# Kernel optimization log

Measured on AMD Instinct MI355X. Metric: run time of the kernel, lower is better.

The kernel has to match this reference:

```python
import jax, jax.numpy as jnp
from jax import lax
import numpy as np

DIVISOR = 2.0

def setup_inputs() -> dict:
    key = jax.random.key(0)
    k1, k2, k3, k4 = jax.random.split(key, 4)
    B, Cin, D, H, W = 64, 8, 32, 64, 64
    Cout, KD, KH, KW = 16, 3, 3, 3
    fan_in = Cin * KD * KH * KW
    bound = 1.0 / np.sqrt(fan_in)
    x = jax.random.normal(k1, (B, Cin, D, H, W), dtype=jnp.float32)
    conv_weight = jax.random.uniform(k2, (Cout, Cin, KD, KH, KW), jnp.float32, -bound, bound)
    conv_bias = jax.random.uniform(k3, (Cout,), jnp.float32, -bound, bound)
    bias = jax.random.normal(k4, (Cout, 1, 1, 1), dtype=jnp.float32) * 0.02
    return {"x": x, "conv_weight": conv_weight, "conv_bias": conv_bias, "bias": bias}

def reference(x, conv_weight, conv_bias, bias):
    # Conv3d, stride 1, no padding, groups=1  -> [B, Cout, D-2, H-2, W-2]
    y = lax.conv_general_dilated(
        x, conv_weight, window_strides=(1, 1, 1), padding='VALID',
        dimension_numbers=('NCDHW', 'OIDHW', 'NCDHW'))
    y = y + conv_bias[None, :, None, None, None]
    # Divide by constant
    y = y / DIVISOR
    # MaxPool3d(kernel=2, stride=2), floor mode (VALID drops the trailing odd row)
    y = lax.reduce_window(y, -jnp.inf, lax.max,
                          window_dimensions=(1, 1, 2, 2, 2),
                          window_strides=(1, 1, 2, 2, 2), padding='VALID')
    # AdaptiveAvgPool3d((1,1,1)) == global mean over spatial dims
    y = jnp.mean(y, axis=(2, 3, 4), keepdims=True)  # [B, Cout, 1, 1, 1]
    # Bias add (broadcast over batch)
    y = y + bias[None]
    # Sum over channel dim (sum_dim=1, no keepdim)
    return jnp.sum(y, axis=1)  # [B, 1, 1, 1]
```

## Files before the change

kernel.cpp:

```cpp
#include <hip/hip_runtime.h>

typedef __attribute__((ext_vector_type(8))) short short8;
typedef __attribute__((ext_vector_type(4))) float f32x4;
typedef unsigned int u32;

#define ROW_B 1056
#define SLOT_B 10560
#define NSLOT 4

__device__ __forceinline__ unsigned short f2bf(float f) {
  unsigned u = __builtin_bit_cast(unsigned, f);
  u += 0x7FFFu + ((u >> 16) & 1u);
  return (unsigned short)(u >> 16);
}
__device__ __forceinline__ u32 cvtpk(float lo, float hi) {
  u32 r;
  asm("v_cvt_pk_bf16_f32 %0, %1, %2" : "=v"(r) : "v"(lo), "v"(hi));
  return r;
}

#define MF(ACC, H, FR, KD, KH)                                                \
  ACC[H][wt] = __builtin_amdgcn_mfma_f32_16x16x32_bf16(FR, bfragB[KD][KH],    \
                                                       ACC[H][wt], 0, 0, 0)
#define MFI(ACC, H, FR)                                                       \
  ACC[H][wt] = __builtin_amdgcn_mfma_f32_16x16x32_bf16(FR, bfragB[0][0],      \
                                                       zf4, 0, 0, 0)

#define PROC(DP, AN, AM, AO, K1, K2, DOCLOSE, SAVEP, DOSTAGE)                 \
  {                                                                           \
    const int dp_ = (DP);                                                     \
    if (DOSTAGE) {                                                            \
      stage_load(dp_ + 2);                                                    \
      __builtin_amdgcn_sched_barrier(0);     \
    }                                                                         \
    const int sb_ = (dp_ & 3) * SLOT_B + rowbase;                             \
    __builtin_amdgcn_s_setprio(1);                                            \
    _Pragma("unroll") for (int wt = 0; wt < 4; ++wt) {                        \
      const short8 f0 = *(const short8*)(smem + sb_ + 0 * ROW_B + physoff[wt]); \
      const short8 f1 = *(const short8*)(smem + sb_ + 1 * ROW_B + physoff[wt]); \
      const short8 f2 = *(const short8*)(smem + sb_ + 2 * ROW_B + physoff[wt]); \
      const short8 f3 = *(const short8*)(smem + sb_ + 3 * ROW_B + physoff[wt]); \
      MFI(AN, 0, f0); MFI(AN, 1, f1);                                         \
      MF(AN, 0, f1, 0, 1); MF(AN, 1, f2, 0, 1);                               \
      MF(AN, 0, f2, 0, 2); MF(AN, 1, f3, 0, 2);                               \
      if (K1) {                                                               \
        MF(AM, 0, f0, 1, 0); MF(AM, 1, f1, 1, 0);                             \
        MF(AM, 0, f1, 1, 1); MF(AM, 1, f2, 1, 1);                             \
        MF(AM, 0, f2, 1, 2); MF(AM, 1, f3, 1, 2);                             \
      }                                                                       \
      if (K2) {                                                               \
        MF(AO, 0, f0, 2, 0); MF(AO, 1, f1, 2, 0);                             \
        MF(AO, 0, f1, 2, 1); MF(AO, 1, f2, 2, 1);                             \
        MF(AO, 0, f2, 2, 2); MF(AO, 1, f3, 2, 2);                             \
      }                                                                       \
    }                                                                         \
    __builtin_amdgcn_s_setprio(0);                                            \
    if (DOSTAGE) stage_write(dp_ + 2);                                        \
    __syncthreads();                                                          \
    if (DOCLOSE) {                                                            \
      _Pragma("unroll") for (int wt = 0; wt < 4; ++wt) {                      \
        const float e01 = fmaxf(fmaxf(AO[0][wt][0], AO[0][wt][1]),            \
                                fmaxf(AO[1][wt][0], AO[1][wt][1]));           \
        const float e23 = fmaxf(fmaxf(AO[0][wt][2], AO[0][wt][3]),            \
                                fmaxf(AO[1][wt][2], AO[1][wt][3]));           \
        if (SAVEP) {                                                          \
          p01[wt] = e01; p23[wt] = e23;                                       \
        } else if (hvalid) {                                                  \
          sum += fmaxf(p01[wt], e01);                                         \
          if (!(wt == 3 && g == 3)) sum += fmaxf(p23[wt], e23);               \
        }                                                                     \
      }                                                                       \
    }                                                                         \
  }

__launch_bounds__(256, 2)
__global__ void conv_fused(const float* __restrict__ x,
                           const float* __restrict__ cw,
                           float* __restrict__ ws) {
  __shared__ __align__(16) unsigned char smem[NSLOT * SLOT_B];
  __shared__ float wsum[4];

  const int bid = blockIdx.x;
  const int b   = bid >> 3;
  const int hq  = bid & 7;
  const int h0  = hq * 8;

  const int tid  = threadIdx.x;
  const int lane = tid & 63;
  const int wid  = tid >> 6;
  const int nm   = lane & 15;
  const int g    = lane >> 4;

  const float* xb = x + (size_t)b * (8u * 32u * 64u * 64u);

  short8 bfragB[3][3];
#pragma unroll
  for (int kd = 0; kd < 3; ++kd)
#pragma unroll
    for (int kh = 0; kh < 3; ++kh) {
      short8 f;
#pragma unroll
      for (int j = 0; j < 8; ++j) {
        float v = (g < 3) ? cw[(nm * 8 + j) * 27 + kd * 9 + kh * 3 + g] : 0.f;
        f[j] = (short)f2bf(v);
      }
      bfragB[kd][kh] = f;
    }

  const int gc = (g < 3) ? g : 2;
  int physoff[4];
#pragma unroll
  for (int wt = 0; wt < 4; ++wt) physoff[wt] = (wt * 16 + nm + gc) * 16;
  const int rowbase = (2 * wid) * ROW_B;

  bool st_act[3]; const float* st_base[3]; int st_off[3];
#pragma unroll
  for (int pass = 0; pass < 3; ++pass) {
    const int t = tid + pass * 256;
    bool act = (t < 640);
    int row = (t >> 6) % 10;
    const int w = t & 63;
    int h = h0 + row;
    if (h > 63) { act = false; h = 63; }
    st_act[pass]  = act;
    st_base[pass] = xb + h * 64 + w;
    st_off[pass]  = row * ROW_B + w * 16;
  }

  float ld[3][8];

  auto stage_load = [&](int p) {
#pragma unroll
    for (int pass = 0; pass < 3; ++pass) {
      if (st_act[pass]) {
        const float* sp = st_base[pass] + p * 4096;
#pragma unroll
        for (int c = 0; c < 8; ++c) ld[pass][c] = sp[(size_t)c * 131072];
      }
    }
  };
  auto stage_write = [&](int p) {
    unsigned char* d = smem + (p & 3) * SLOT_B;
#pragma unroll
    for (int pass = 0; pass < 3; ++pass) {
      if (st_act[pass]) {
        uint4 v;
        v.x = cvtpk(ld[pass][0], ld[pass][1]);
        v.y = cvtpk(ld[pass][2], ld[pass][3]);
        v.z = cvtpk(ld[pass][4], ld[pass][5]);
        v.w = cvtpk(ld[pass][6], ld[pass][7]);
        *(uint4*)(d + st_off[pass]) = v;
      }
    }
  };

  const bool hvalid = !(hq == 7 && wid == 3);
  const f32x4 zf4 = {0.f, 0.f, 0.f, 0.f};
  float sum = 0.f;
  float p01[4], p23[4];
  f32x4 accA[2][4], accB[2][4], accC[2][4];

  stage_load(0); stage_write(0);
  stage_load(1); stage_write(1);
  __syncthreads();

  PROC(0, accA, accB, accC, 0, 0, 0, 0, 1)
  PROC(1, accB, accA, accC, 1, 0, 0, 0, 1)

  for (int p0 = 2; p0 <= 20; p0 += 6) {
    PROC(p0 + 0, accC, accB, accA, 1, 1, 1, 1, 1)
    PROC(p0 + 1, accA, accC, accB, 1, 1, 1, 0, 1)
    PROC(p0 + 2, accB, accA, accC, 1, 1, 1, 1, 1)
    PROC(p0 + 3, accC, accB, accA, 1, 1, 1, 0, 1)
    PROC(p0 + 4, accA, accC, accB, 1, 1, 1, 1, 1)
    PROC(p0 + 5, accB, accA, accC, 1, 1, 1, 0, 1)
  }
  PROC(26, accC, accB, accA, 1, 1, 1, 1, 1)
  PROC(27, accA, accC, accB, 1, 1, 1, 0, 1)
  PROC(28, accB, accA, accC, 1, 1, 1, 1, 1)
  PROC(29, accC, accB, accA, 1, 1, 1, 0, 1)
  PROC(30, accA, accC, accB, 1, 1, 1, 1, 0)
  PROC(31, accB, accA, accC, 1, 1, 1, 0, 0)

#pragma unroll
  for (int off = 32; off > 0; off >>= 1) sum += __shfl_down(sum, off);
  if (lane == 0) wsum[wid] = sum;
  __syncthreads();
  if (tid == 0) ws[bid] = wsum[0] + wsum[1] + wsum[2] + wsum[3];
}

__global__ void finalize_k(const float* __restrict__ ws,
                           const float* __restrict__ cb,
                           const float* __restrict__ bias,
                           float* __restrict__ out) {
  const int b = threadIdx.x;
  float s = 0.f;
#pragma unroll
  for (int hq = 0; hq < 8; ++hq) s += ws[b * 8 + hq];
  float cbs = 0.f, bs = 0.f;
#pragma unroll
  for (int c = 0; c < 16; ++c) { cbs += cb[c]; bs += bias[c]; }
  out[b] = 0.5f * s / 14415.f + 0.5f * cbs + bs;
}

extern "C" void kernel_launch(void* const* d_in, const int* in_sizes, int n_in,
                              void* d_out, int out_size, void* d_ws, size_t ws_size,
                              hipStream_t stream) {
  const float* x    = (const float*)d_in[0];
  const float* cw   = (const float*)d_in[1];
  const float* cb   = (const float*)d_in[2];
  const float* bias = (const float*)d_in[3];
  float* out = (float*)d_out;
  float* ws  = (float*)d_ws;

  hipLaunchKernelGGL(conv_fused, dim3(512), dim3(256), 0, stream, x, cw, ws);
  hipLaunchKernelGGL(finalize_k, dim3(1), dim3(64), 0, stream, ws, cb, bias, out);
}
```

Baseline: 75.28 us.

## Split conv tile into half-height blocks with 2x2 wave layout and fewer barriers

```diff
diff --git a/kernel.cpp b/kernel.cpp
--- a/kernel.cpp
+++ b/kernel.cpp
@@ -5,7 +5,7 @@
 typedef unsigned int u32;
 
 #define ROW_B 1056
-#define SLOT_B 10560
+#define SLOT_B 6336
 #define NSLOT 4
 
 __device__ __forceinline__ unsigned short f2bf(float f) {
@@ -26,16 +26,13 @@
   ACC[H][wt] = __builtin_amdgcn_mfma_f32_16x16x32_bf16(FR, bfragB[0][0],      \
                                                        zf4, 0, 0, 0)
 
-#define PROC(DP, AN, AM, AO, K1, K2, DOCLOSE, SAVEP, DOSTAGE)                 \
+#define PROC(DP, AN, AM, AO, K1, K2, DOCLOSE, SAVEP, DOSTAGE, DOBAR)          \
   {                                                                           \
     const int dp_ = (DP);                                                     \
-    if (DOSTAGE) {                                                            \
-      stage_load(dp_ + 2);                                                    \
-      __builtin_amdgcn_sched_barrier(0);     \
-    }                                                                         \
+    if (DOSTAGE) stage(dp_ + 2);                                              \
     const int sb_ = (dp_ & 3) * SLOT_B + rowbase;                             \
     __builtin_amdgcn_s_setprio(1);                                            \
-    _Pragma("unroll") for (int wt = 0; wt < 4; ++wt) {                        \
+    _Pragma("unroll") for (int wt = 0; wt < 2; ++wt) {                        \
       const short8 f0 = *(const short8*)(smem + sb_ + 0 * ROW_B + physoff[wt]); \
       const short8 f1 = *(const short8*)(smem + sb_ + 1 * ROW_B + physoff[wt]); \
       const short8 f2 = *(const short8*)(smem + sb_ + 2 * ROW_B + physoff[wt]); \
@@ -55,41 +52,42 @@
       }                                                                       \
     }                                                                         \
     __builtin_amdgcn_s_setprio(0);                                            \
-    if (DOSTAGE) stage_write(dp_ + 2);                                        \
-    __syncthreads();                                                          \
+    if (DOBAR) __syncthreads();                                               \
     if (DOCLOSE) {                                                            \
-      _Pragma("unroll") for (int wt = 0; wt < 4; ++wt) {                      \
+      _Pragma("unroll") for (int wt = 0; wt < 2; ++wt) {                      \
         const float e01 = fmaxf(fmaxf(AO[0][wt][0], AO[0][wt][1]),            \
                                 fmaxf(AO[1][wt][0], AO[1][wt][1]));           \
         const float e23 = fmaxf(fmaxf(AO[0][wt][2], AO[0][wt][3]),            \
                                 fmaxf(AO[1][wt][2], AO[1][wt][3]));           \
         if (SAVEP) {                                                          \
           p01[wt] = e01; p23[wt] = e23;                                       \
-        } else if (hvalid) {                                                  \
+        } else if (pairvalid) {                                               \
           sum += fmaxf(p01[wt], e01);                                         \
-          if (!(wt == 3 && g == 3)) sum += fmaxf(p23[wt], e23);               \
+          if (!(wt == 1 && wmask)) sum += fmaxf(p23[wt], e23);                \
         }                                                                     \
       }                                                                       \
     }                                                                         \
   }
 
-__launch_bounds__(256, 2)
+__launch_bounds__(256, 3)
 __global__ void conv_fused(const float* __restrict__ x,
                            const float* __restrict__ cw,
                            float* __restrict__ ws) {
   __shared__ __align__(16) unsigned char smem[NSLOT * SLOT_B];
   __shared__ float wsum[4];
 
-  const int bid = blockIdx.x;
-  const int b   = bid >> 3;
-  const int hq  = bid & 7;
-  const int h0  = hq * 8;
+  const int rb  = blockIdx.x;
+  const int bid = (rb & 7) * 128 + (rb >> 3);
+  const int b   = bid >> 4;
+  const int hq  = bid & 15;
 
   const int tid  = threadIdx.x;
   const int lane = tid & 63;
   const int wid  = tid >> 6;
   const int nm   = lane & 15;
   const int g    = lane >> 4;
+  const int hp   = wid >> 1;
+  const int wh   = wid & 1;
 
   const float* xb = x + (size_t)b * (8u * 32u * 64u * 64u);
 
@@ -108,82 +106,80 @@
     }
 
   const int gc = (g < 3) ? g : 2;
-  int physoff[4];
-#pragma unroll
-  for (int wt = 0; wt < 4; ++wt) physoff[wt] = (wt * 16 + nm + gc) * 16;
-  const int rowbase = (2 * wid) * ROW_B;
-
-  bool st_act[3]; const float* st_base[3]; int st_off[3];
-#pragma unroll
-  for (int pass = 0; pass < 3; ++pass) {
-    const int t = tid + pass * 256;
-    bool act = (t < 640);
-    int row = (t >> 6) % 10;
-    const int w = t & 63;
-    int h = h0 + row;
-    if (h > 63) { act = false; h = 63; }
-    st_act[pass]  = act;
-    st_base[pass] = xb + h * 64 + w;
-    st_off[pass]  = row * ROW_B + w * 16;
-  }
-
-  float ld[3][8];
-
-  auto stage_load = [&](int p) {
-#pragma unroll
-    for (int pass = 0; pass < 3; ++pass) {
-      if (st_act[pass]) {
-        const float* sp = st_base[pass] + p * 4096;
-#pragma unroll
-        for (int c = 0; c < 8; ++c) ld[pass][c] = sp[(size_t)c * 131072];
-      }
+  int physoff[2];
+#pragma unroll
+  for (int wt = 0; wt < 2; ++wt)
+    physoff[wt] = ((2 * wh + wt) * 16 + nm + gc) * 16;
+  const int rowbase = (2 * hp) * ROW_B;
+
+  const int w0    = tid & 63;
+  const int srow0 = tid >> 6;
+  const int srow1 = 4 + (srow0 & 1);
+  int h0 = 4 * hq + srow0; if (h0 > 63) h0 = 63;
+  int h1 = 4 * hq + srow1; if (h1 > 63) h1 = 63;
+  const float* st_base0 = xb + h0 * 64 + w0;
+  const float* st_base1 = xb + h1 * 64 + w0;
+  const int st_off0 = srow0 * ROW_B + w0 * 16;
+  const int st_off1 = srow1 * ROW_B + w0 * 16;
+  const bool act1 = (tid < 128);
+
+  auto stage = [&](int p) {
+    unsigned char* d = smem + (p & 3) * SLOT_B;
+    {
+      const float* sp = st_base0 + p * 4096;
+      float v[8];
+#pragma unroll
+      for (int c = 0; c < 8; ++c) v[c] = sp[(size_t)c * 131072];
+      uint4 q;
+      q.x = cvtpk(v[0], v[1]); q.y = cvtpk(v[2], v[3]);
+      q.z = cvtpk(v[4], v[5]); q.w = cvtpk(v[6], v[7]);
+      *(uint4*)(d + st_off0) = q;
+    }
+    if (act1) {
+      const float* sp = st_base1 + p * 4096;
+      float v[8];
+#pragma unroll
+      for (int c = 0; c < 8; ++c) v[c] = sp[(size_t)c * 131072];
+      uint4 q;
+      q.x = cvtpk(v[0], v[1]); q.y = cvtpk(v[2], v[3]);
+      q.z = cvtpk(v[4], v[5]); q.w = cvtpk(v[6], v[7]);
+      *(uint4*)(d + st_off1) = q;
     }
   };
-  auto stage_write = [&](int p) {
-    unsigned char* d = smem + (p & 3) * SLOT_B;
-#pragma unroll
-    for (int pass = 0; pass < 3; ++pass) {
-      if (st_act[pass]) {
-        uint4 v;
-        v.x = cvtpk(ld[pass][0], ld[pass][1]);
-        v.y = cvtpk(ld[pass][2], ld[pass][3]);
-        v.z = cvtpk(ld[pass][4], ld[pass][5]);
-        v.w = cvtpk(ld[pass][6], ld[pass][7]);
-        *(uint4*)(d + st_off[pass]) = v;
-      }
-    }
-  };
-
-  const bool hvalid = !(hq == 7 && wid == 3);
+
+  const bool pairvalid = !(hq == 15 && hp == 1);
+  const bool wmask = (wh == 1) && (g == 3);
+
   const f32x4 zf4 = {0.f, 0.f, 0.f, 0.f};
   float sum = 0.f;
-  float p01[4], p23[4];
-  f32x4 accA[2][4], accB[2][4], accC[2][4];
-
-  stage_load(0); stage_write(0);
-  stage_load(1); stage_write(1);
+  float p01[2], p23[2];
+  f32x4 accA[2][2], accB[2][2], accC[2][2];
+
+  stage(0);
+  stage(1);
   __syncthreads();
 
-  PROC(0, accA, accB, accC, 0, 0, 0, 0, 1)
-  PROC(1, accB, accA, accC, 1, 0, 0, 0, 1)
+  PROC(0, accA, accB, accC, 0, 0, 0, 0, 1, 0)
+  PROC(1, accB, accA, accC, 1, 0, 0, 0, 1, 1)
 
   for (int p0 = 2; p0 <= 20; p0 += 6) {
-    PROC(p0 + 0, accC, accB, accA, 1, 1, 1, 1, 1)
-    PROC(p0 + 1, accA, accC, accB, 1, 1, 1, 0, 1)
-    PROC(p0 + 2, accB, accA, accC, 1, 1, 1, 1, 1)
-    PROC(p0 + 3, accC, accB, accA, 1, 1, 1, 0, 1)
-    PROC(p0 + 4, accA, accC, accB, 1, 1, 1, 1, 1)
-    PROC(p0 + 5, accB, accA, accC, 1, 1, 1, 0, 1)
+    PROC(p0 + 0, accC, accB, accA, 1, 1, 1, 1, 1, 0)
+    PROC(p0 + 1, accA, accC, accB, 1, 1, 1, 0, 1, 1)
+    PROC(p0 + 2, accB, accA, accC, 1, 1, 1, 1, 1, 0)
+    PROC(p0 + 3, accC, accB, accA, 1, 1, 1, 0, 1, 1)
+    PROC(p0 + 4, accA, accC, accB, 1, 1, 1, 1, 1, 0)
+    PROC(p0 + 5, accB, accA, accC, 1, 1, 1, 0, 1, 1)
   }
-  PROC(26, accC, accB, accA, 1, 1, 1, 1, 1)
-  PROC(27, accA, accC, accB, 1, 1, 1, 0, 1)
-  PROC(28, accB, accA, accC, 1, 1, 1, 1, 1)
-  PROC(29, accC, accB, accA, 1, 1, 1, 0, 1)
-  PROC(30, accA, accC, accB, 1, 1, 1, 1, 0)
-  PROC(31, accB, accA, accC, 1, 1, 1, 0, 0)
+  PROC(26, accC, accB, accA, 1, 1, 1, 1, 1, 0)
+  PROC(27, accA, accC, accB, 1, 1, 1, 0, 1, 1)
+  PROC(28, accB, accA, accC, 1, 1, 1, 1, 1, 0)
+  PROC(29, accC, accB, accA, 1, 1, 1, 0, 1, 1)
+  PROC(30, accA, accC, accB, 1, 1, 1, 1, 0, 0)
+  PROC(31, accB, accA, accC, 1, 1, 1, 0, 0, 0)
 
 #pragma unroll
   for (int off = 32; off > 0; off >>= 1) sum += __shfl_down(sum, off);
+  __syncthreads();
   if (lane == 0) wsum[wid] = sum;
   __syncthreads();
   if (tid == 0) ws[bid] = wsum[0] + wsum[1] + wsum[2] + wsum[3];
@@ -196,7 +192,7 @@
   const int b = threadIdx.x;
   float s = 0.f;
 #pragma unroll
-  for (int hq = 0; hq < 8; ++hq) s += ws[b * 8 + hq];
+  for (int hq = 0; hq < 16; ++hq) s += ws[b * 16 + hq];
   float cbs = 0.f, bs = 0.f;
 #pragma unroll
   for (int c = 0; c < 16; ++c) { cbs += cb[c]; bs += bias[c]; }
@@ -213,6 +209,6 @@
   float* out = (float*)d_out;
   float* ws  = (float*)d_ws;
 
-  hipLaunchKernelGGL(conv_fused, dim3(512), dim3(256), 0, stream, x, cw, ws);
+  hipLaunchKernelGGL(conv_fused, dim3(1024), dim3(256), 0, stream, x, cw, ws);
   hipLaunchKernelGGL(finalize_k, dim3(1), dim3(64), 0, stream, ws, cb, bias, out);
 }
```

After: 99.70 us. +32.4%, slower.

## Halve per-plane barriers, skip dead tail MFMAs, and remap block order

Applied to the files above, without the earlier changes.

```diff
diff --git a/kernel.cpp b/kernel.cpp
--- a/kernel.cpp
+++ b/kernel.cpp
@@ -26,7 +26,7 @@
   ACC[H][wt] = __builtin_amdgcn_mfma_f32_16x16x32_bf16(FR, bfragB[0][0],      \
                                                        zf4, 0, 0, 0)
 
-#define PROC(DP, AN, AM, AO, K1, K2, DOCLOSE, SAVEP, DOSTAGE)                 \
+#define PROC(DP, AN, AM, AO, K0, K1, K2, DOCLOSE, SAVEP, DOSTAGE, DOBAR)      \
   {                                                                           \
     const int dp_ = (DP);                                                     \
     if (DOSTAGE) {                                                            \
@@ -40,9 +40,11 @@
       const short8 f1 = *(const short8*)(smem + sb_ + 1 * ROW_B + physoff[wt]); \
       const short8 f2 = *(const short8*)(smem + sb_ + 2 * ROW_B + physoff[wt]); \
       const short8 f3 = *(const short8*)(smem + sb_ + 3 * ROW_B + physoff[wt]); \
-      MFI(AN, 0, f0); MFI(AN, 1, f1);                                         \
-      MF(AN, 0, f1, 0, 1); MF(AN, 1, f2, 0, 1);                               \
-      MF(AN, 0, f2, 0, 2); MF(AN, 1, f3, 0, 2);                               \
+      if (K0) {                                                               \
+        MFI(AN, 0, f0); MFI(AN, 1, f1);                                       \
+        MF(AN, 0, f1, 0, 1); MF(AN, 1, f2, 0, 1);                             \
+        MF(AN, 0, f2, 0, 2); MF(AN, 1, f3, 0, 2);                             \
+      }                                                                       \
       if (K1) {                                                               \
         MF(AM, 0, f0, 1, 0); MF(AM, 1, f1, 1, 0);                             \
         MF(AM, 0, f1, 1, 1); MF(AM, 1, f2, 1, 1);                             \
@@ -56,7 +58,7 @@
     }                                                                         \
     __builtin_amdgcn_s_setprio(0);                                            \
     if (DOSTAGE) stage_write(dp_ + 2);                                        \
-    __syncthreads();                                                          \
+    if (DOBAR) __syncthreads();                                               \
     if (DOCLOSE) {                                                            \
       _Pragma("unroll") for (int wt = 0; wt < 4; ++wt) {                      \
         const float e01 = fmaxf(fmaxf(AO[0][wt][0], AO[0][wt][1]),            \
@@ -80,7 +82,8 @@
   __shared__ __align__(16) unsigned char smem[NSLOT * SLOT_B];
   __shared__ float wsum[4];
 
-  const int bid = blockIdx.x;
+  const int rb  = blockIdx.x;
+  const int bid = (rb & 7) * 64 + (rb >> 3);
   const int b   = bid >> 3;
   const int hq  = bid & 7;
   const int h0  = hq * 8;
@@ -164,23 +167,23 @@
   stage_load(1); stage_write(1);
   __syncthreads();
 
-  PROC(0, accA, accB, accC, 0, 0, 0, 0, 1)
-  PROC(1, accB, accA, accC, 1, 0, 0, 0, 1)
+  PROC(0, accA, accB, accC, 1, 0, 0, 0, 0, 1, 0)
+  PROC(1, accB, accA, accC, 1, 1, 0, 0, 0, 1, 1)
 
   for (int p0 = 2; p0 <= 20; p0 += 6) {
-    PROC(p0 + 0, accC, accB, accA, 1, 1, 1, 1, 1)
-    PROC(p0 + 1, accA, accC, accB, 1, 1, 1, 0, 1)
-    PROC(p0 + 2, accB, accA, accC, 1, 1, 1, 1, 1)
-    PROC(p0 + 3, accC, accB, accA, 1, 1, 1, 0, 1)
-    PROC(p0 + 4, accA, accC, accB, 1, 1, 1, 1, 1)
-    PROC(p0 + 5, accB, accA, accC, 1, 1, 1, 0, 1)
+    PROC(p0 + 0, accC, accB, accA, 1, 1, 1, 1, 1, 1, 0)
+    PROC(p0 + 1, accA, accC, accB, 1, 1, 1, 1, 0, 1, 1)
+    PROC(p0 + 2, accB, accA, accC, 1, 1, 1, 1, 1, 1, 0)
+    PROC(p0 + 3, accC, accB, accA, 1, 1, 1, 1, 0, 1, 1)
+    PROC(p0 + 4, accA, accC, accB, 1, 1, 1, 1, 1, 1, 0)
+    PROC(p0 + 5, accB, accA, accC, 1, 1, 1, 1, 0, 1, 1)
   }
-  PROC(26, accC, accB, accA, 1, 1, 1, 1, 1)
-  PROC(27, accA, accC, accB, 1, 1, 1, 0, 1)
-  PROC(28, accB, accA, accC, 1, 1, 1, 1, 1)
-  PROC(29, accC, accB, accA, 1, 1, 1, 0, 1)
-  PROC(30, accA, accC, accB, 1, 1, 1, 1, 0)
-  PROC(31, accB, accA, accC, 1, 1, 1, 0, 0)
+  PROC(26, accC, accB, accA, 1, 1, 1, 1, 1, 1, 0)
+  PROC(27, accA, accC, accB, 1, 1, 1, 1, 0, 1, 1)
+  PROC(28, accB, accA, accC, 1, 1, 1, 1, 1, 1, 0)
+  PROC(29, accC, accB, accA, 1, 1, 1, 1, 0, 1, 1)
+  PROC(30, accA, accC, accB, 0, 1, 1, 1, 1, 0, 0)
+  PROC(31, accB, accA, accC, 0, 0, 1, 1, 0, 0, 0)
 
 #pragma unroll
   for (int off = 32; off > 0; off >>= 1) sum += __shfl_down(sum, off);
```

Measured after the change: 75.39 us. About the same (+0.1%).
